# Performance work log

Measured on AMD Instinct MI355X. Metric: run time of the kernel, lower is better.

Reference implementation:

```python
import jax, jax.numpy as jnp
import numpy as np


def setup_inputs() -> dict:
    key = jax.random.key(0)
    k1, k2, k3, k4 = jax.random.split(key, 4)
    N, F, E, M = 50000, 128, 1600000, 1024
    return {
        "molec_feature_vectures": jax.random.normal(k1, (N, F), dtype=jnp.float32),
        "W": jax.random.normal(k2, (F, F), dtype=jnp.float32),
        "mo_neighbour_indices": jax.random.randint(k3, (2, E), 0, N, dtype=jnp.int64),
        "mo_mol_id": jax.random.randint(k4, (E,), 0, M, dtype=jnp.int64),
        "n_output": M,
    }


def reference(molec_feature_vectures, W, mo_neighbour_indices, mo_mol_id, n_output):
    # Gather endpoint features for each neighbor pair: [E, F]
    fi = molec_feature_vectures[mo_neighbour_indices[0]]
    fj = molec_feature_vectures[mo_neighbour_indices[1]]
    # Symmetric bilinear form (mode='pes'): s_n = fi_n . (W + W^T) . fj_n
    Ws = W + W.T  # [F, F]
    # Fuse as (fi @ Ws) * fj summed over F to avoid a 3-operand einsum blowup
    scalars = jnp.einsum('ni,ij,nj->n', fi, Ws, fj)  # [E]
    # Segment-sum per molecule
    res = jax.ops.segment_sum(scalars, mo_mol_id, num_segments=n_output)  # [M]
    return res
```

## Files before the change

kernel.cpp:

```cpp
#include <hip/hip_runtime.h>
#include <hip/hip_bf16.h>

#define FDIM 128
#define BROWS 32
#define NBLK 256

typedef __attribute__((ext_vector_type(8))) short short8v;
typedef __attribute__((ext_vector_type(4))) float f32x4;

static __device__ __forceinline__ unsigned short f2bf(float x) {
    unsigned u = __float_as_uint(x);
    unsigned r = 0x7fffu + ((u >> 16) & 1u);
    return (unsigned short)((u + r) >> 16);
}
static __device__ __forceinline__ float bf2f(unsigned short h) {
    return __uint_as_float((unsigned)h << 16);
}

static __device__ __forceinline__ void split2(float v, short& h, short& l) {
    unsigned short hh = f2bf(v);
    h = (short)hh;
    l = (short)f2bf(v - bf2f(hh));
}

__global__ __launch_bounds__(512, 4) void gemm_mfma(
    const float* __restrict__ Fm, const float* __restrict__ W,
    unsigned short* __restrict__ Gbf, int N) {
    __shared__ unsigned short sH[128 * 136];
    __shared__ unsigned short sL[128 * 136];

    for (int idx = threadIdx.x; idx < 128 * 128; idx += 512) {
        int i = idx >> 7, j = idx & 127;
        float w = W[idx] + W[j * 128 + i];
        short h, l;
        split2(w, h, l);
        sH[i * 136 + j] = (unsigned short)h;
        sL[i * 136 + j] = (unsigned short)l;
    }
    __syncthreads();

    const int wid  = threadIdx.x >> 6;
    const int lane = threadIdx.x & 63;
    const int ar   = lane & 15;
    const int kg   = lane >> 4;
    const int row0 = blockIdx.x * 128 + wid * 16;
    const int gr   = row0 + ar;
    const bool rv  = gr < N;
    const float* fp = Fm + (size_t)gr * FDIM;

    f32x4 acc[8];
#pragma unroll
    for (int t = 0; t < 8; ++t) acc[t] = (f32x4){0.f, 0.f, 0.f, 0.f};

#pragma unroll
    for (int ks = 0; ks < 4; ++ks) {
        const int k0 = ks * 32 + kg * 8;
        float4 fa = make_float4(0.f, 0.f, 0.f, 0.f);
        float4 fb = make_float4(0.f, 0.f, 0.f, 0.f);
        if (rv) {
            fa = *(const float4*)(fp + k0);
            fb = *(const float4*)(fp + k0 + 4);
        }
        short8v ah, al;
        {
            short h, l;
            split2(fa.x, h, l); ah[0] = h; al[0] = l;
            split2(fa.y, h, l); ah[1] = h; al[1] = l;
            split2(fa.z, h, l); ah[2] = h; al[2] = l;
            split2(fa.w, h, l); ah[3] = h; al[3] = l;
            split2(fb.x, h, l); ah[4] = h; al[4] = l;
            split2(fb.y, h, l); ah[5] = h; al[5] = l;
            split2(fb.z, h, l); ah[6] = h; al[6] = l;
            split2(fb.w, h, l); ah[7] = h; al[7] = l;
        }
#pragma unroll
        for (int ct = 0; ct < 8; ++ct) {
            const short8v bh = *(const short8v*)(sH + (ct * 16 + ar) * 136 + k0);
            const short8v bl = *(const short8v*)(sL + (ct * 16 + ar) * 136 + k0);
            acc[ct] = __builtin_amdgcn_mfma_f32_16x16x32_bf16(ah, bh, acc[ct], 0, 0, 0);
            acc[ct] = __builtin_amdgcn_mfma_f32_16x16x32_bf16(ah, bl, acc[ct], 0, 0, 0);
            acc[ct] = __builtin_amdgcn_mfma_f32_16x16x32_bf16(al, bh, acc[ct], 0, 0, 0);
        }
    }

#pragma unroll
    for (int r = 0; r < 4; ++r) {
        const int orow = row0 + kg * 4 + r;
        if (orow < N) {
#pragma unroll
            for (int ct = 0; ct < 8; ++ct)
                Gbf[(size_t)orow * FDIM + ct * 16 + ar] = f2bf(acc[ct][r]);
        }
    }
}

__global__ __launch_bounds__(256) void k_hist(const int* __restrict__ idx, int E,
                                              int nb, unsigned* __restrict__ M,
                                              float* __restrict__ out, int Mout) {
    if (blockIdx.x == 0) {
        for (int i = threadIdx.x; i < Mout; i += 256) out[i] = 0.f;
    }
    extern __shared__ unsigned cnt[];
    for (int i = threadIdx.x; i < nb; i += 256) cnt[i] = 0;
    __syncthreads();
    int chunk = (E + NBLK - 1) / NBLK;
    int s = blockIdx.x * chunk;
    int e_end = min(E, s + chunk);
    for (int e = s + threadIdx.x; e < e_end; e += 256) {
        int i1 = idx[E + e];
        atomicAdd(&cnt[i1 >> 5], 1u);
    }
    __syncthreads();
    for (int i = threadIdx.x; i < nb; i += 256)
        M[(size_t)blockIdx.x * nb + i] = cnt[i];
}

__global__ __launch_bounds__(256) void k_mscan2(unsigned* __restrict__ M, int nb,
                                                unsigned* __restrict__ tot) {
    int b = blockIdx.x * 4 + (threadIdx.x >> 6);
    int lane = threadIdx.x & 63;
    if (b >= nb) return;
    unsigned m0 = M[(size_t)(4 * lane + 0) * nb + b];
    unsigned m1 = M[(size_t)(4 * lane + 1) * nb + b];
    unsigned m2 = M[(size_t)(4 * lane + 2) * nb + b];
    unsigned m3 = M[(size_t)(4 * lane + 3) * nb + b];
    unsigned s = m0 + m1 + m2 + m3;
    unsigned incl = s;
#pragma unroll
    for (int d = 1; d < 64; d <<= 1) {
        unsigned u = __shfl_up(incl, d, 64);
        if (lane >= d) incl += u;
    }
    unsigned run = incl - s;
    M[(size_t)(4 * lane + 0) * nb + b] = run; run += m0;
    M[(size_t)(4 * lane + 1) * nb + b] = run; run += m1;
    M[(size_t)(4 * lane + 2) * nb + b] = run; run += m2;
    M[(size_t)(4 * lane + 3) * nb + b] = run;
    if (lane == 63) tot[b] = incl;
}

__global__ __launch_bounds__(256) void k_bscan(const unsigned* __restrict__ tot, int nb,
                                               unsigned* __restrict__ bucketStart) {
    __shared__ unsigned wS[4];
    int t = threadIdx.x;
    unsigned v0, v1, v2, v3, v4, v5, v6, v7;
    int b0 = t * 8;
    v0 = (b0 + 0 < nb) ? tot[b0 + 0] : 0u;
    v1 = (b0 + 1 < nb) ? tot[b0 + 1] : 0u;
    v2 = (b0 + 2 < nb) ? tot[b0 + 2] : 0u;
    v3 = (b0 + 3 < nb) ? tot[b0 + 3] : 0u;
    v4 = (b0 + 4 < nb) ? tot[b0 + 4] : 0u;
    v5 = (b0 + 5 < nb) ? tot[b0 + 5] : 0u;
    v6 = (b0 + 6 < nb) ? tot[b0 + 6] : 0u;
    v7 = (b0 + 7 < nb) ? tot[b0 + 7] : 0u;
    unsigned l0 = 0, l1 = v0, l2 = l1 + v1, l3 = l2 + v2, l4 = l3 + v3,
             l5 = l4 + v4, l6 = l5 + v5, l7 = l6 + v6;
    unsigned s = l7 + v7;
    int lane = t & 63, wid = t >> 6;
    unsigned incl = s;
    for (int d = 1; d < 64; d <<= 1) {
        unsigned u = __shfl_up(incl, d, 64);
        if (lane >= d) incl += u;
    }
    if (lane == 63) wS[wid] = incl;
    __syncthreads();
    unsigned wOff = 0;
    for (int i = 0; i < wid; ++i) wOff += wS[i];
    unsigned base = wOff + incl - s;
    if (b0 + 0 < nb) bucketStart[b0 + 0] = base + l0;
    if (b0 + 1 < nb) bucketStart[b0 + 1] = base + l1;
    if (b0 + 2 < nb) bucketStart[b0 + 2] = base + l2;
    if (b0 + 3 < nb) bucketStart[b0 + 3] = base + l3;
    if (b0 + 4 < nb) bucketStart[b0 + 4] = base + l4;
    if (b0 + 5 < nb) bucketStart[b0 + 5] = base + l5;
    if (b0 + 6 < nb) bucketStart[b0 + 6] = base + l6;
    if (b0 + 7 < nb) bucketStart[b0 + 7] = base + l7;
    if (t == 255) bucketStart[nb] = base + s;
}

__global__ __launch_bounds__(256) void k_scatter(const int* __restrict__ idx,
                                                 const int* __restrict__ mol, int E,
                                                 int nb, const unsigned* __restrict__ M,
                                                 const unsigned* __restrict__ bucketStart,
                                                 unsigned* __restrict__ sortedE) {
    extern __shared__ unsigned cur[];
    for (int i = threadIdx.x; i < nb; i += 256)
        cur[i] = M[(size_t)blockIdx.x * nb + i] + bucketStart[i];
    __syncthreads();
    int chunk = (E + NBLK - 1) / NBLK;
    int s = blockIdx.x * chunk;
    int e_end = min(E, s + chunk);
    for (int e = s + threadIdx.x; e < e_end; e += 256) {
        int i0 = idx[e];
        int i1 = idx[E + e];
        int m  = mol[e];
        int b  = i1 >> 5;
        int loc = i1 & 31;
        unsigned pos = atomicAdd(&cur[b], 1u);
        sortedE[pos] = (unsigned)i0 | ((unsigned)m << 16) | ((unsigned)loc << 26);
    }
}

__global__ __launch_bounds__(512, 8) void edge_kernel(
    const unsigned short* __restrict__ Gbf, const float* __restrict__ Fm,
    const unsigned* __restrict__ sortedE, const unsigned* __restrict__ bucketStart,
    float* __restrict__ out, int N, int Mout) {
    __shared__ __align__(16) unsigned short sFrow[BROWS * FDIM];
    __shared__ float smol[1024];

    const int b = blockIdx.x;
    const int row0 = b * BROWS;
    const int nrow = min(BROWS, N - row0);

    for (int k = threadIdx.x; k < nrow * 16; k += 512) {
        int r = k >> 4, g = k & 15;
        const float4* src = (const float4*)(Fm + (size_t)(row0 + r) * FDIM + g * 8);
        float4 v0 = src[0], v1 = src[1];
        unsigned u0 = (unsigned)f2bf(v0.x) | ((unsigned)f2bf(v0.y) << 16);
        unsigned u1 = (unsigned)f2bf(v0.z) | ((unsigned)f2bf(v0.w) << 16);
        unsigned u2 = (unsigned)f2bf(v1.x) | ((unsigned)f2bf(v1.y) << 16);
        unsigned u3 = (unsigned)f2bf(v1.z) | ((unsigned)f2bf(v1.w) << 16);
        char* dst = (char*)sFrow + r * 256 + ((g * 16) ^ ((r & 7) << 4));
        *(uint4*)dst = make_uint4(u0, u1, u2, u3);
    }
    for (int i = threadIdx.x; i < 1024; i += 512) smol[i] = 0.f;
    __syncthreads();

    const int s = (int)bucketStart[b];
    const int e_end = (int)bucketStart[b + 1];
    const int lane = threadIdx.x & 63;
    const int wid  = threadIdx.x >> 6;
    const int er = lane & 15;
    const int kg = lane >> 4;
    const bool isdiag = ((er >> 2) == kg);

    int base = s + wid * 16;
    unsigned pk = 0u;
    if (base + er < e_end && base < e_end) pk = sortedE[base + er];

    while (base < e_end) {
        const int nbase = base + 128;
        unsigned npk = 0u;
        if (nbase < e_end && nbase + er < e_end) npk = sortedE[nbase + er];

        const int i0  = pk & 0xffff;
        const int loc = pk >> 26;
        const unsigned short* gp = Gbf + (size_t)i0 * FDIM + kg * 8;
        const char* lp = (const char*)sFrow + loc * 256;
        const int swz = (loc & 7) << 4;

        f32x4 acc = (f32x4){0.f, 0.f, 0.f, 0.f};
#pragma unroll
        for (int ks = 0; ks < 4; ++ks) {
            short8v a  = *(const short8v*)(gp + ks * 32);
            short8v bf = *(const short8v*)(lp + ((ks * 64 + kg * 16) ^ swz));
            acc = __builtin_amdgcn_mfma_f32_16x16x32_bf16(a, bf, acc, 0, 0, 0);
        }
        if (isdiag && (base + er < e_end)) {
            atomicAdd(&smol[(pk >> 16) & 0x3ff], acc[er & 3]);
        }
        pk = npk;
        base = nbase;
    }
    __syncthreads();

    for (int i = threadIdx.x; i < Mout; i += 512) {
        float v = smol[i];
        if (v != 0.f) atomicAdd(&out[i], v);
    }
}

extern "C" void kernel_launch(void* const* d_in, const int* in_sizes, int n_in,
                              void* d_out, int out_size, void* d_ws, size_t ws_size,
                              hipStream_t stream) {
    const float* Fm = (const float*)d_in[0];
    const float* W  = (const float*)d_in[1];
    const int* idx  = (const int*)d_in[2];
    const int* mol  = (const int*)d_in[3];
    float* out = (float*)d_out;

    const int N = in_sizes[0] / FDIM;
    const int E = in_sizes[3];

    const int nb = (N + BROWS - 1) / BROWS;

    char* ws = (char*)d_ws;
    size_t o = 0;
    unsigned short* Gbf = (unsigned short*)(ws + o); o += ((size_t)N * FDIM * 2 + 255) & ~(size_t)255;
    unsigned* sortedE = (unsigned*)(ws + o);         o += ((size_t)E * 4 + 255) & ~(size_t)255;
    unsigned* M = (unsigned*)(ws + o);               o += ((size_t)NBLK * nb * 4 + 255) & ~(size_t)255;
    unsigned* tot = (unsigned*)(ws + o);             o += ((size_t)nb * 4 + 255) & ~(size_t)255;
    unsigned* bucketStart = (unsigned*)(ws + o);     o += ((size_t)(nb + 1) * 4 + 255) & ~(size_t)255;

    gemm_mfma<<<(N + 127) / 128, 512, 0, stream>>>(Fm, W, Gbf, N);

    size_t smem = (size_t)nb * 4;
    k_hist<<<NBLK, 256, smem, stream>>>(idx, E, nb, M, out, out_size);
    k_mscan2<<<(nb + 3) / 4, 256, 0, stream>>>(M, nb, tot);
    k_bscan<<<1, 256, 0, stream>>>(tot, nb, bucketStart);
    k_scatter<<<NBLK, 256, smem, stream>>>(idx, mol, E, nb, M, bucketStart, sortedE);

    edge_kernel<<<nb, 512, 0, stream>>>(Gbf, Fm, sortedE, bucketStart, out, N, out_size);
}
```

Baseline: 210.5 us.

## Hold bucket rows in registers, prefetch gathers, precompute Ws once, widen sort grid

The edge kernel now keeps all 32 bucket rows of B fragments in registers and computes two MFMA tiles per 16-edge group. This removes the per-edge swizzled LDS reads, and lanes pick the right diagonal element through shuffles. Gathered G rows are software-prefetched one iteration ahead, and the block shrinks to 256 threads. The symmetric W split into bf16 hi/lo moves to a separate tiny kernel instead of running in every GEMM block. The histogram and scatter grids double to 512 blocks, and the scan reads eight entries per lane. The cost is more register pressure from the prefetched A fragments and two accumulators, and twice as many MFMAs per edge, half of which are wasted.

```diff
diff --git a/kernel.cpp b/kernel.cpp
--- a/kernel.cpp
+++ b/kernel.cpp
@@ -3,7 +3,7 @@
 
 #define FDIM 128
 #define BROWS 32
-#define NBLK 256
+#define NBLK 512
 
 typedef __attribute__((ext_vector_type(8))) short short8v;
 typedef __attribute__((ext_vector_type(4))) float f32x4;
@@ -23,19 +23,31 @@
     l = (short)f2bf(v - bf2f(hh));
 }
 
+__global__ void make_ws2(const float* __restrict__ W,
+                         unsigned short* __restrict__ WsH,
+                         unsigned short* __restrict__ WsL) {
+    int idx = blockIdx.x * 256 + threadIdx.x;
+    int i = idx >> 7, j = idx & 127;
+    float w = W[idx] + W[j * 128 + i];
+    short h, l;
+    split2(w, h, l);
+    WsH[idx] = (unsigned short)h;
+    WsL[idx] = (unsigned short)l;
+}
+
 __global__ __launch_bounds__(512, 4) void gemm_mfma(
-    const float* __restrict__ Fm, const float* __restrict__ W,
+    const float* __restrict__ Fm,
+    const unsigned short* __restrict__ WsH, const unsigned short* __restrict__ WsL,
     unsigned short* __restrict__ Gbf, int N) {
-    __shared__ unsigned short sH[128 * 136];
-    __shared__ unsigned short sL[128 * 136];
-
-    for (int idx = threadIdx.x; idx < 128 * 128; idx += 512) {
-        int i = idx >> 7, j = idx & 127;
-        float w = W[idx] + W[j * 128 + i];
-        short h, l;
-        split2(w, h, l);
-        sH[i * 136 + j] = (unsigned short)h;
-        sL[i * 136 + j] = (unsigned short)l;
+    __shared__ __align__(16) unsigned short sH[128 * 136];
+    __shared__ __align__(16) unsigned short sL[128 * 136];
+
+    for (int k = threadIdx.x; k < 128 * 16; k += 512) {
+        int i = k >> 4, g = k & 15;
+        *(uint4*)((char*)sH + i * 272 + g * 16) =
+            *(const uint4*)((const char*)WsH + i * 256 + g * 16);
+        *(uint4*)((char*)sL + i * 272 + g * 16) =
+            *(const uint4*)((const char*)WsL + i * 256 + g * 16);
     }
     __syncthreads();
 
@@ -120,11 +132,13 @@
     int b = blockIdx.x * 4 + (threadIdx.x >> 6);
     int lane = threadIdx.x & 63;
     if (b >= nb) return;
-    unsigned m0 = M[(size_t)(4 * lane + 0) * nb + b];
-    unsigned m1 = M[(size_t)(4 * lane + 1) * nb + b];
-    unsigned m2 = M[(size_t)(4 * lane + 2) * nb + b];
-    unsigned m3 = M[(size_t)(4 * lane + 3) * nb + b];
-    unsigned s = m0 + m1 + m2 + m3;
+    unsigned m[8];
+    unsigned s = 0;
+#pragma unroll
+    for (int j = 0; j < 8; ++j) {
+        m[j] = M[(size_t)(8 * lane + j) * nb + b];
+        s += m[j];
+    }
     unsigned incl = s;
 #pragma unroll
     for (int d = 1; d < 64; d <<= 1) {
@@ -132,10 +146,11 @@
         if (lane >= d) incl += u;
     }
     unsigned run = incl - s;
-    M[(size_t)(4 * lane + 0) * nb + b] = run; run += m0;
-    M[(size_t)(4 * lane + 1) * nb + b] = run; run += m1;
-    M[(size_t)(4 * lane + 2) * nb + b] = run; run += m2;
-    M[(size_t)(4 * lane + 3) * nb + b] = run;
+#pragma unroll
+    for (int j = 0; j < 8; ++j) {
+        M[(size_t)(8 * lane + j) * nb + b] = run;
+        run += m[j];
+    }
     if (lane == 63) tot[b] = incl;
 }
 
@@ -201,18 +216,18 @@
     }
 }
 
-__global__ __launch_bounds__(512, 8) void edge_kernel(
+__global__ __launch_bounds__(256, 5) void edge_kernel(
     const unsigned short* __restrict__ Gbf, const float* __restrict__ Fm,
     const unsigned* __restrict__ sortedE, const unsigned* __restrict__ bucketStart,
     float* __restrict__ out, int N, int Mout) {
-    __shared__ __align__(16) unsigned short sFrow[BROWS * FDIM];
+    __shared__ __align__(16) unsigned short sFw[BROWS * 136];
     __shared__ float smol[1024];
 
     const int b = blockIdx.x;
     const int row0 = b * BROWS;
     const int nrow = min(BROWS, N - row0);
 
-    for (int k = threadIdx.x; k < nrow * 16; k += 512) {
+    for (int k = threadIdx.x; k < nrow * 16; k += 256) {
         int r = k >> 4, g = k & 15;
         const float4* src = (const float4*)(Fm + (size_t)(row0 + r) * FDIM + g * 8);
         float4 v0 = src[0], v1 = src[1];
@@ -220,51 +235,73 @@
         unsigned u1 = (unsigned)f2bf(v0.z) | ((unsigned)f2bf(v0.w) << 16);
         unsigned u2 = (unsigned)f2bf(v1.x) | ((unsigned)f2bf(v1.y) << 16);
         unsigned u3 = (unsigned)f2bf(v1.z) | ((unsigned)f2bf(v1.w) << 16);
-        char* dst = (char*)sFrow + r * 256 + ((g * 16) ^ ((r & 7) << 4));
-        *(uint4*)dst = make_uint4(u0, u1, u2, u3);
-    }
-    for (int i = threadIdx.x; i < 1024; i += 512) smol[i] = 0.f;
-    __syncthreads();
-
-    const int s = (int)bucketStart[b];
-    const int e_end = (int)bucketStart[b + 1];
+        *(uint4*)((char*)sFw + r * 272 + g * 16) = make_uint4(u0, u1, u2, u3);
+    }
+    for (int i = threadIdx.x; i < 1024; i += 256) smol[i] = 0.f;
+    __syncthreads();
+
     const int lane = threadIdx.x & 63;
     const int wid  = threadIdx.x >> 6;
     const int er = lane & 15;
     const int kg = lane >> 4;
-    const bool isdiag = ((er >> 2) == kg);
+
+    short8v Bf0[4], Bf1[4];
+#pragma unroll
+    for (int ks = 0; ks < 4; ++ks) {
+        Bf0[ks] = *(const short8v*)((char*)sFw + er * 272 + ks * 64 + kg * 16);
+        Bf1[ks] = *(const short8v*)((char*)sFw + (16 + er) * 272 + ks * 64 + kg * 16);
+    }
+
+    const int s = (int)bucketStart[b];
+    const int e_end = (int)bucketStart[b + 1];
 
     int base = s + wid * 16;
     unsigned pk = 0u;
-    if (base + er < e_end && base < e_end) pk = sortedE[base + er];
+    if (base + er < e_end) pk = sortedE[base + er];
+    const unsigned short* gp = Gbf + (size_t)(pk & 0xffff) * FDIM + kg * 8;
+    short8v a0 = *(const short8v*)(gp);
+    short8v a1 = *(const short8v*)(gp + 32);
+    short8v a2 = *(const short8v*)(gp + 64);
+    short8v a3 = *(const short8v*)(gp + 96);
 
     while (base < e_end) {
-        const int nbase = base + 128;
+        const int nbase = base + 64;
         unsigned npk = 0u;
-        if (nbase < e_end && nbase + er < e_end) npk = sortedE[nbase + er];
-
-        const int i0  = pk & 0xffff;
-        const int loc = pk >> 26;
-        const unsigned short* gp = Gbf + (size_t)i0 * FDIM + kg * 8;
-        const char* lp = (const char*)sFrow + loc * 256;
-        const int swz = (loc & 7) << 4;
-
-        f32x4 acc = (f32x4){0.f, 0.f, 0.f, 0.f};
-#pragma unroll
-        for (int ks = 0; ks < 4; ++ks) {
-            short8v a  = *(const short8v*)(gp + ks * 32);
-            short8v bf = *(const short8v*)(lp + ((ks * 64 + kg * 16) ^ swz));
-            acc = __builtin_amdgcn_mfma_f32_16x16x32_bf16(a, bf, acc, 0, 0, 0);
-        }
-        if (isdiag && (base + er < e_end)) {
-            atomicAdd(&smol[(pk >> 16) & 0x3ff], acc[er & 3]);
-        }
+        if (nbase + er < e_end) npk = sortedE[nbase + er];
+        const unsigned short* ngp = Gbf + (size_t)(npk & 0xffff) * FDIM + kg * 8;
+        short8v na0 = *(const short8v*)(ngp);
+        short8v na1 = *(const short8v*)(ngp + 32);
+        short8v na2 = *(const short8v*)(ngp + 64);
+        short8v na3 = *(const short8v*)(ngp + 96);
+
+        f32x4 acc0 = (f32x4){0.f, 0.f, 0.f, 0.f};
+        f32x4 acc1 = (f32x4){0.f, 0.f, 0.f, 0.f};
+        acc0 = __builtin_amdgcn_mfma_f32_16x16x32_bf16(a0, Bf0[0], acc0, 0, 0, 0);
+        acc1 = __builtin_amdgcn_mfma_f32_16x16x32_bf16(a0, Bf1[0], acc1, 0, 0, 0);
+        acc0 = __builtin_amdgcn_mfma_f32_16x16x32_bf16(a1, Bf0[1], acc0, 0, 0, 0);
+        acc1 = __builtin_amdgcn_mfma_f32_16x16x32_bf16(a1, Bf1[1], acc1, 0, 0, 0);
+        acc0 = __builtin_amdgcn_mfma_f32_16x16x32_bf16(a2, Bf0[2], acc0, 0, 0, 0);
+        acc1 = __builtin_amdgcn_mfma_f32_16x16x32_bf16(a2, Bf1[2], acc1, 0, 0, 0);
+        acc0 = __builtin_amdgcn_mfma_f32_16x16x32_bf16(a3, Bf0[3], acc0, 0, 0, 0);
+        acc1 = __builtin_amdgcn_mfma_f32_16x16x32_bf16(a3, Bf1[3], acc1, 0, 0, 0);
+
+#pragma unroll
+        for (int r = 0; r < 4; ++r) {
+            const int ej = ((lane >> 4) << 2) | r;
+            unsigned epk = __shfl(pk, ej, 64);
+            int locr = (int)(epk >> 26);
+            if ((base + ej < e_end) && ((locr & 15) == er)) {
+                float v = (locr & 16) ? acc1[r] : acc0[r];
+                atomicAdd(&smol[(epk >> 16) & 0x3ff], v);
+            }
+        }
+        a0 = na0; a1 = na1; a2 = na2; a3 = na3;
         pk = npk;
         base = nbase;
     }
     __syncthreads();
 
-    for (int i = threadIdx.x; i < Mout; i += 512) {
+    for (int i = threadIdx.x; i < Mout; i += 256) {
         float v = smol[i];
         if (v != 0.f) atomicAdd(&out[i], v);
     }
@@ -286,13 +323,16 @@
 
     char* ws = (char*)d_ws;
     size_t o = 0;
+    unsigned short* WsH = (unsigned short*)(ws + o); o += 32 * 1024;
+    unsigned short* WsL = (unsigned short*)(ws + o); o += 32 * 1024;
     unsigned short* Gbf = (unsigned short*)(ws + o); o += ((size_t)N * FDIM * 2 + 255) & ~(size_t)255;
     unsigned* sortedE = (unsigned*)(ws + o);         o += ((size_t)E * 4 + 255) & ~(size_t)255;
     unsigned* M = (unsigned*)(ws + o);               o += ((size_t)NBLK * nb * 4 + 255) & ~(size_t)255;
     unsigned* tot = (unsigned*)(ws + o);             o += ((size_t)nb * 4 + 255) & ~(size_t)255;
     unsigned* bucketStart = (unsigned*)(ws + o);     o += ((size_t)(nb + 1) * 4 + 255) & ~(size_t)255;
 
-    gemm_mfma<<<(N + 127) / 128, 512, 0, stream>>>(Fm, W, Gbf, N);
+    make_ws2<<<64, 256, 0, stream>>>(W, WsH, WsL);
+    gemm_mfma<<<(N + 127) / 128, 512, 0, stream>>>(Fm, WsH, WsL, Gbf, N);
 
     size_t smem = (size_t)nb * 4;
     k_hist<<<NBLK, 256, smem, stream>>>(idx, E, nb, M, out, out_size);
@@ -300,5 +340,5 @@
     k_bscan<<<1, 256, 0, stream>>>(tot, nb, bucketStart);
     k_scatter<<<NBLK, 256, smem, stream>>>(idx, mol, E, nb, M, bucketStart, sortedE);
 
-    edge_kernel<<<nb, 512, 0, stream>>>(Gbf, Fm, sortedE, bucketStart, out, N, out_size);
-}
+    edge_kernel<<<nb, 256, 0, stream>>>(Gbf, Fm, sortedE, bucketStart, out, N, out_size);
+}
```

Result: slower. 232.7 us (+10.6%).

## Replace bucketed MFMA edge kernel with flat gather dot-product over sorted edges

Applied to the files above, without the earlier changes.

The edge kernel no longer stages a 32-row bf16 tile of the destination features in shared memory or uses MFMA. Each 16-lane group now gathers a bf16 G row and an fp32 F row per edge and reduces the dot product with shuffles, over an even split of edges across 2048 blocks. The sorted edge record grows to 8 bytes so it can carry the full destination index. W+W^T is precomputed into split bf16 buffers by a separate kernel, and the histogram/scatter use 128 blocks of 1024 threads. This drops the per-bucket staging and load imbalance but doubles sortedE traffic and moves fj reads to random fp32 global gathers.

```diff
diff --git a/kernel.cpp b/kernel.cpp
--- a/kernel.cpp
+++ b/kernel.cpp
@@ -3,7 +3,7 @@
 
 #define FDIM 128
 #define BROWS 32
-#define NBLK 256
+#define NBLK 128
 
 typedef __attribute__((ext_vector_type(8))) short short8v;
 typedef __attribute__((ext_vector_type(4))) float f32x4;
@@ -16,6 +16,8 @@
 static __device__ __forceinline__ float bf2f(unsigned short h) {
     return __uint_as_float((unsigned)h << 16);
 }
+static __device__ __forceinline__ float bf_lo(unsigned u) { return __uint_as_float(u << 16); }
+static __device__ __forceinline__ float bf_hi(unsigned u) { return __uint_as_float(u & 0xffff0000u); }
 
 static __device__ __forceinline__ void split2(float v, short& h, short& l) {
     unsigned short hh = f2bf(v);
@@ -23,19 +25,31 @@
     l = (short)f2bf(v - bf2f(hh));
 }
 
+__global__ void make_ws2(const float* __restrict__ W,
+                         unsigned short* __restrict__ WsH,
+                         unsigned short* __restrict__ WsL) {
+    int idx = blockIdx.x * 256 + threadIdx.x;
+    int i = idx >> 7, j = idx & 127;
+    float w = W[idx] + W[j * 128 + i];
+    short h, l;
+    split2(w, h, l);
+    WsH[idx] = (unsigned short)h;
+    WsL[idx] = (unsigned short)l;
+}
+
 __global__ __launch_bounds__(512, 4) void gemm_mfma(
-    const float* __restrict__ Fm, const float* __restrict__ W,
+    const float* __restrict__ Fm,
+    const unsigned short* __restrict__ WsH, const unsigned short* __restrict__ WsL,
     unsigned short* __restrict__ Gbf, int N) {
-    __shared__ unsigned short sH[128 * 136];
-    __shared__ unsigned short sL[128 * 136];
-
-    for (int idx = threadIdx.x; idx < 128 * 128; idx += 512) {
-        int i = idx >> 7, j = idx & 127;
-        float w = W[idx] + W[j * 128 + i];
-        short h, l;
-        split2(w, h, l);
-        sH[i * 136 + j] = (unsigned short)h;
-        sL[i * 136 + j] = (unsigned short)l;
+    __shared__ __align__(16) unsigned short sH[128 * 136];
+    __shared__ __align__(16) unsigned short sL[128 * 136];
+
+    for (int k = threadIdx.x; k < 128 * 16; k += 512) {
+        int i = k >> 4, g = k & 15;
+        *(uint4*)((char*)sH + i * 272 + g * 16) =
+            *(const uint4*)((const char*)WsH + i * 256 + g * 16);
+        *(uint4*)((char*)sL + i * 272 + g * 16) =
+            *(const uint4*)((const char*)WsL + i * 256 + g * 16);
     }
     __syncthreads();
 
@@ -94,24 +108,24 @@
     }
 }
 
-__global__ __launch_bounds__(256) void k_hist(const int* __restrict__ idx, int E,
-                                              int nb, unsigned* __restrict__ M,
-                                              float* __restrict__ out, int Mout) {
+__global__ __launch_bounds__(1024) void k_hist(const int* __restrict__ idx, int E,
+                                               int nb, unsigned* __restrict__ M,
+                                               float* __restrict__ out, int Mout) {
     if (blockIdx.x == 0) {
-        for (int i = threadIdx.x; i < Mout; i += 256) out[i] = 0.f;
+        for (int i = threadIdx.x; i < Mout; i += 1024) out[i] = 0.f;
     }
     extern __shared__ unsigned cnt[];
-    for (int i = threadIdx.x; i < nb; i += 256) cnt[i] = 0;
+    for (int i = threadIdx.x; i < nb; i += 1024) cnt[i] = 0;
     __syncthreads();
     int chunk = (E + NBLK - 1) / NBLK;
     int s = blockIdx.x * chunk;
     int e_end = min(E, s + chunk);
-    for (int e = s + threadIdx.x; e < e_end; e += 256) {
+    for (int e = s + threadIdx.x; e < e_end; e += 1024) {
         int i1 = idx[E + e];
         atomicAdd(&cnt[i1 >> 5], 1u);
     }
     __syncthreads();
-    for (int i = threadIdx.x; i < nb; i += 256)
+    for (int i = threadIdx.x; i < nb; i += 1024)
         M[(size_t)blockIdx.x * nb + i] = cnt[i];
 }
 
@@ -120,11 +134,9 @@
     int b = blockIdx.x * 4 + (threadIdx.x >> 6);
     int lane = threadIdx.x & 63;
     if (b >= nb) return;
-    unsigned m0 = M[(size_t)(4 * lane + 0) * nb + b];
-    unsigned m1 = M[(size_t)(4 * lane + 1) * nb + b];
-    unsigned m2 = M[(size_t)(4 * lane + 2) * nb + b];
-    unsigned m3 = M[(size_t)(4 * lane + 3) * nb + b];
-    unsigned s = m0 + m1 + m2 + m3;
+    unsigned m0 = M[(size_t)(2 * lane + 0) * nb + b];
+    unsigned m1 = M[(size_t)(2 * lane + 1) * nb + b];
+    unsigned s = m0 + m1;
     unsigned incl = s;
 #pragma unroll
     for (int d = 1; d < 64; d <<= 1) {
@@ -132,10 +144,8 @@
         if (lane >= d) incl += u;
     }
     unsigned run = incl - s;
-    M[(size_t)(4 * lane + 0) * nb + b] = run; run += m0;
-    M[(size_t)(4 * lane + 1) * nb + b] = run; run += m1;
-    M[(size_t)(4 * lane + 2) * nb + b] = run; run += m2;
-    M[(size_t)(4 * lane + 3) * nb + b] = run;
+    M[(size_t)(2 * lane + 0) * nb + b] = run; run += m0;
+    M[(size_t)(2 * lane + 1) * nb + b] = run;
     if (lane == 63) tot[b] = incl;
 }
 
@@ -178,89 +188,101 @@
     if (t == 255) bucketStart[nb] = base + s;
 }
 
-__global__ __launch_bounds__(256) void k_scatter(const int* __restrict__ idx,
-                                                 const int* __restrict__ mol, int E,
-                                                 int nb, const unsigned* __restrict__ M,
-                                                 const unsigned* __restrict__ bucketStart,
-                                                 unsigned* __restrict__ sortedE) {
+__global__ __launch_bounds__(1024) void k_scatter(const int* __restrict__ idx,
+                                                  const int* __restrict__ mol, int E,
+                                                  int nb, const unsigned* __restrict__ M,
+                                                  const unsigned* __restrict__ bucketStart,
+                                                  uint2* __restrict__ sortedE) {
     extern __shared__ unsigned cur[];
-    for (int i = threadIdx.x; i < nb; i += 256)
+    for (int i = threadIdx.x; i < nb; i += 1024)
         cur[i] = M[(size_t)blockIdx.x * nb + i] + bucketStart[i];
     __syncthreads();
     int chunk = (E + NBLK - 1) / NBLK;
     int s = blockIdx.x * chunk;
     int e_end = min(E, s + chunk);
-    for (int e = s + threadIdx.x; e < e_end; e += 256) {
+    for (int e = s + threadIdx.x; e < e_end; e += 1024) {
         int i0 = idx[e];
         int i1 = idx[E + e];
         int m  = mol[e];
         int b  = i1 >> 5;
-        int loc = i1 & 31;
         unsigned pos = atomicAdd(&cur[b], 1u);
-        sortedE[pos] = (unsigned)i0 | ((unsigned)m << 16) | ((unsigned)loc << 26);
+        sortedE[pos] = make_uint2((unsigned)i0 | ((unsigned)m << 16), (unsigned)i1);
     }
 }
 
 __global__ __launch_bounds__(512, 8) void edge_kernel(
     const unsigned short* __restrict__ Gbf, const float* __restrict__ Fm,
-    const unsigned* __restrict__ sortedE, const unsigned* __restrict__ bucketStart,
-    float* __restrict__ out, int N, int Mout) {
-    __shared__ __align__(16) unsigned short sFrow[BROWS * FDIM];
+    const uint2* __restrict__ sortedE, int E,
+    float* __restrict__ out, int Mout) {
     __shared__ float smol[1024];
 
-    const int b = blockIdx.x;
-    const int row0 = b * BROWS;
-    const int nrow = min(BROWS, N - row0);
-
-    for (int k = threadIdx.x; k < nrow * 16; k += 512) {
-        int r = k >> 4, g = k & 15;
-        const float4* src = (const float4*)(Fm + (size_t)(row0 + r) * FDIM + g * 8);
-        float4 v0 = src[0], v1 = src[1];
-        unsigned u0 = (unsigned)f2bf(v0.x) | ((unsigned)f2bf(v0.y) << 16);
-        unsigned u1 = (unsigned)f2bf(v0.z) | ((unsigned)f2bf(v0.w) << 16);
-        unsigned u2 = (unsigned)f2bf(v1.x) | ((unsigned)f2bf(v1.y) << 16);
-        unsigned u3 = (unsigned)f2bf(v1.z) | ((unsigned)f2bf(v1.w) << 16);
-        char* dst = (char*)sFrow + r * 256 + ((g * 16) ^ ((r & 7) << 4));
-        *(uint4*)dst = make_uint4(u0, u1, u2, u3);
-    }
     for (int i = threadIdx.x; i < 1024; i += 512) smol[i] = 0.f;
     __syncthreads();
 
-    const int s = (int)bucketStart[b];
-    const int e_end = (int)bucketStart[b + 1];
+    const int nchunk = (E + (int)gridDim.x - 1) / (int)gridDim.x;
+    const int s = blockIdx.x * nchunk;
+    const int e_end = min(E, s + nchunk);
+
     const int lane = threadIdx.x & 63;
+    const int sub  = lane >> 4;
+    const int t16  = lane & 15;
+    const int off16 = t16 * 8;
     const int wid  = threadIdx.x >> 6;
-    const int er = lane & 15;
-    const int kg = lane >> 4;
-    const bool isdiag = ((er >> 2) == kg);
-
-    int base = s + wid * 16;
-    unsigned pk = 0u;
-    if (base + er < e_end && base < e_end) pk = sortedE[base + er];
+
+    int base = s + wid * 8;
+    uint2 pkA = make_uint2(0u, 0u), pkB = make_uint2(0u, 0u);
+    if (base + sub < e_end)     pkA = sortedE[base + sub];
+    if (base + 4 + sub < e_end) pkB = sortedE[base + 4 + sub];
 
     while (base < e_end) {
-        const int nbase = base + 128;
-        unsigned npk = 0u;
-        if (nbase < e_end && nbase + er < e_end) npk = sortedE[nbase + er];
-
-        const int i0  = pk & 0xffff;
-        const int loc = pk >> 26;
-        const unsigned short* gp = Gbf + (size_t)i0 * FDIM + kg * 8;
-        const char* lp = (const char*)sFrow + loc * 256;
-        const int swz = (loc & 7) << 4;
-
-        f32x4 acc = (f32x4){0.f, 0.f, 0.f, 0.f};
-#pragma unroll
-        for (int ks = 0; ks < 4; ++ks) {
-            short8v a  = *(const short8v*)(gp + ks * 32);
-            short8v bf = *(const short8v*)(lp + ((ks * 64 + kg * 16) ^ swz));
-            acc = __builtin_amdgcn_mfma_f32_16x16x32_bf16(a, bf, acc, 0, 0, 0);
-        }
-        if (isdiag && (base + er < e_end)) {
-            atomicAdd(&smol[(pk >> 16) & 0x3ff], acc[er & 3]);
-        }
-        pk = npk;
-        base = nbase;
+        const int nbase = base + 64;
+        uint2 npkA = make_uint2(0u, 0u), npkB = make_uint2(0u, 0u);
+        if (nbase + sub < e_end)     npkA = sortedE[nbase + sub];
+        if (nbase + 4 + sub < e_end) npkB = sortedE[nbase + 4 + sub];
+
+        const bool vA = (base + sub) < e_end;
+        const bool vB = (base + 4 + sub) < e_end;
+        const uint4 gA = *(const uint4*)(Gbf + (size_t)(pkA.x & 0xffff) * FDIM + off16);
+        const uint4 gB = *(const uint4*)(Gbf + (size_t)(pkB.x & 0xffff) * FDIM + off16);
+        const float* fpA = Fm + (size_t)pkA.y * FDIM + off16;
+        const float* fpB = Fm + (size_t)pkB.y * FDIM + off16;
+        const float4 fA0 = *(const float4*)(fpA);
+        const float4 fA1 = *(const float4*)(fpA + 4);
+        const float4 fB0 = *(const float4*)(fpB);
+        const float4 fB1 = *(const float4*)(fpB + 4);
+
+        float pA, pB;
+        pA = bf_lo(gA.x) * fA0.x;
+        pA = fmaf(bf_hi(gA.x), fA0.y, pA);
+        pA = fmaf(bf_lo(gA.y), fA0.z, pA);
+        pA = fmaf(bf_hi(gA.y), fA0.w, pA);
+        pA = fmaf(bf_lo(gA.z), fA1.x, pA);
+        pA = fmaf(bf_hi(gA.z), fA1.y, pA);
+        pA = fmaf(bf_lo(gA.w), fA1.z, pA);
+        pA = fmaf(bf_hi(gA.w), fA1.w, pA);
+        pB = bf_lo(gB.x) * fB0.x;
+        pB = fmaf(bf_hi(gB.x), fB0.y, pB);
+        pB = fmaf(bf_lo(gB.y), fB0.z, pB);
+        pB = fmaf(bf_hi(gB.y), fB0.w, pB);
+        pB = fmaf(bf_lo(gB.z), fB1.x, pB);
+        pB = fmaf(bf_hi(gB.z), fB1.y, pB);
+        pB = fmaf(bf_lo(gB.w), fB1.z, pB);
+        pB = fmaf(bf_hi(gB.w), fB1.w, pB);
+
+        pA += __shfl_xor(pA, 1, 16);
+        pB += __shfl_xor(pB, 1, 16);
+        pA += __shfl_xor(pA, 2, 16);
+        pB += __shfl_xor(pB, 2, 16);
+        pA += __shfl_xor(pA, 4, 16);
+        pB += __shfl_xor(pB, 4, 16);
+        pA += __shfl_xor(pA, 8, 16);
+        pB += __shfl_xor(pB, 8, 16);
+
+        if (t16 == 0) {
+            if (vA) atomicAdd(&smol[pkA.x >> 16], pA);
+            if (vB) atomicAdd(&smol[pkB.x >> 16], pB);
+        }
+        pkA = npkA; pkB = npkB; base = nbase;
     }
     __syncthreads();
 
@@ -286,19 +308,22 @@
 
     char* ws = (char*)d_ws;
     size_t o = 0;
+    unsigned short* WsH = (unsigned short*)(ws + o); o += 32 * 1024;
+    unsigned short* WsL = (unsigned short*)(ws + o); o += 32 * 1024;
     unsigned short* Gbf = (unsigned short*)(ws + o); o += ((size_t)N * FDIM * 2 + 255) & ~(size_t)255;
-    unsigned* sortedE = (unsigned*)(ws + o);         o += ((size_t)E * 4 + 255) & ~(size_t)255;
+    uint2* sortedE = (uint2*)(ws + o);               o += ((size_t)E * 8 + 255) & ~(size_t)255;
     unsigned* M = (unsigned*)(ws + o);               o += ((size_t)NBLK * nb * 4 + 255) & ~(size_t)255;
     unsigned* tot = (unsigned*)(ws + o);             o += ((size_t)nb * 4 + 255) & ~(size_t)255;
     unsigned* bucketStart = (unsigned*)(ws + o);     o += ((size_t)(nb + 1) * 4 + 255) & ~(size_t)255;
 
-    gemm_mfma<<<(N + 127) / 128, 512, 0, stream>>>(Fm, W, Gbf, N);
+    make_ws2<<<64, 256, 0, stream>>>(W, WsH, WsL);
+    gemm_mfma<<<(N + 127) / 128, 512, 0, stream>>>(Fm, WsH, WsL, Gbf, N);
 
     size_t smem = (size_t)nb * 4;
-    k_hist<<<NBLK, 256, smem, stream>>>(idx, E, nb, M, out, out_size);
+    k_hist<<<NBLK, 1024, smem, stream>>>(idx, E, nb, M, out, out_size);
     k_mscan2<<<(nb + 3) / 4, 256, 0, stream>>>(M, nb, tot);
     k_bscan<<<1, 256, 0, stream>>>(tot, nb, bucketStart);
-    k_scatter<<<NBLK, 256, smem, stream>>>(idx, mol, E, nb, M, bucketStart, sortedE);
-
-    edge_kernel<<<nb, 512, 0, stream>>>(Gbf, Fm, sortedE, bucketStart, out, N, out_size);
-}
+    k_scatter<<<NBLK, 1024, smem, stream>>>(idx, mol, E, nb, M, bucketStart, sortedE);
+
+    edge_kernel<<<2048, 512, 0, stream>>>(Gbf, Fm, sortedE, E, out, out_size);
+}
```

Result: no change. 206.8 us (-1.7%).
